# Kernel optimization log

Hardware: AMD Instinct MI355X
Metric: run time of the kernel (lower is better)

The kernel has to match this reference:

```python
import jax, jax.numpy as jnp
import numpy as np

N, K, C0, H = 256, 16, 16, 32  # vertices, regular degree, input feats, hidden


def setup_inputs() -> dict:
    key = jax.random.key(0)
    ks = jax.random.split(key, 4)
    # k-regular circulant graph: neighbors of i are i+/-1..i+/-K//2 (mod N), sorted by vertex id
    offs = np.concatenate([np.arange(1, K // 2 + 1), -np.arange(1, K // 2 + 1)])
    nbrs = np.sort((np.arange(N)[:, None] + offs[None, :]) % N, axis=1).astype(np.int32)
    X = jax.random.normal(ks[0], (N, C0), jnp.float32)
    W1 = jax.random.normal(ks[1], (18 * C0, H), jnp.float32) / np.sqrt(18 * C0)
    b1 = jnp.zeros((H,), jnp.float32)
    W2 = jax.random.normal(ks[2], (18 * H, H), jnp.float32) / np.sqrt(18 * H)
    b2 = jnp.zeros((H,), jnp.float32)
    fc_w = jax.random.normal(ks[3], (H, 1), jnp.float32) / np.sqrt(H)
    fc_b = jnp.zeros((1,), jnp.float32)
    return {"X": X, "nbrs": jnp.asarray(nbrs), "W1": W1, "b1": b1,
            "W2": W2, "b2": b2, "fc_w": fc_w, "fc_b": fc_b}


def contract18(T, A):
    """All 18 contractions of F6[t,a,b,e,f,c] = T[t,a,b,c] * A[e,f],
    exactly matching _collapse6to3 (_c6to2_111 + _c6to2_12 + _c6to2_3),
    without materializing the 6-d tensor.
    T: (n, k, k, k, c) with axes (vertex, t, a, b, channel); A: (k, k).
    Returns (n, k, k, 18*c)."""
    S = A.sum()            # total sum of A
    r = A.sum(1)           # row sums
    tr = jnp.trace(A)
    sum_b = T.sum(3)              # (n,t,a,c)
    sum_t = T.sum(1)              # (n,a,b,c)
    sum_ab = T.sum((2, 3))        # (n,t,c)
    sum_tb = T.sum((1, 3))        # (n,a,c)
    sum_all = T.sum((1, 2, 3))    # (n,c)
    # _c6to2_111 (5 permutations)
    c1 = sum_b * S
    c2 = sum_ab[:, :, None, :] * r[None, None, :, None]
    c3 = sum_t * S
    c4 = sum_tb[:, :, None, :] * r[None, None, :, None]
    c5 = sum_all[:, None, None, :] * A[None, :, :, None]
    # _c6to2_12 (1 nontrivial permutation + 9 identical identity permutations)
    c6 = jnp.einsum('ntabc,b->ntac', T, r)
    c7 = sum_b * tr  # repeated 9 times, as in the source
    # _c6to2_3 (3 planar-diagonal contractions)
    d_ab = jnp.diagonal(T, axis1=2, axis2=3).transpose(0, 1, 3, 2)   # (n,t,a,c): T[t,a,a,c]
    c16 = jnp.einsum('ntac,ea->ntec', d_ab, A)
    d_tb = jnp.diagonal(T, axis1=1, axis2=3)                          # (n,a,c,t): T[t,a,t,c]
    c17 = jnp.einsum('nact,et->naec', d_tb, A)
    d_ttt = jnp.einsum('ntttc->ntc', T).sum(1)                        # (n,c)
    c18 = d_ttt[:, None, None, :] * A[None, :, :, None]
    return jnp.concatenate([c1, c2, c3, c4, c5, c6] + [c7] * 9 + [c16, c17, c18], axis=-1)


def _forward(X, nbrs, W1, b1, W2, b2, fc_w, fc_b):
    n, k = nbrs.shape
    # chi_{i,t}[a,p] = 1 iff a-th neighbor of i == p-th neighbor of j, j = nbrs[i,t]
    NN = nbrs[nbrs]                                                    # (n,k,k)
    CH = (nbrs[:, None, :, None] == NN[:, :, None, :]).astype(X.dtype)  # (n,t,a,p)
    A = jnp.eye(k, dtype=X.dtype)  # chi_{i,i} is the k x k identity for every i

    # get_F0: broadcast vertex features to (n, k, k, c0)
    F = jnp.broadcast_to(X[:, None, None, :], (n, k, k, X.shape[1]))

    def layer(F, W, b):
        Fg = F[nbrs]                                             # (n,t,p,q,c) gather neighbor features
        tmp = jnp.einsum('ntap,ntpqc->ntaqc', CH, Fg)            # chi @ F
        T = jnp.einsum('ntaqc,ntbq->ntabc', tmp, CH)             # (chi @ F) @ chi^T
        col = contract18(T, A)                                   # (n,k,k,18c)
        return jax.nn.relu(col @ W + b)

    F1 = layer(F, W1, b1)
    F2 = layer(F1, W2, b2)
    # get_Troot then full sum: chi_root scatters F2 entries injectively into [n,n,c],
    # so sum over Troot == sum over all entries of F2.
    g = F2.sum((0, 1, 2))                                        # (H,)
    return g @ fc_w + fc_b                                       # (1,)


def reference(X, nbrs, W1, b1, W2, b2, fc_w, fc_b):
    return _forward(X, nbrs, W1, b1, W2, b2, fc_w, fc_b)
```

## Files before the change

kernel.cpp:

```cpp
#include <hip/hip_runtime.h>


constexpr int KN = 16, HH = 32, NV = 256, C2 = 32;

__device__ __forceinline__ float rlane(float v, int l) {
    return __int_as_float(__builtin_amdgcn_readlane(__float_as_int(v), l));
}

#define MM_RL(WPTR, NB, COEF_EXPR, ACC) do {                                   \
    _Pragma("unroll")                                                          \
    for (int B = 0; B < (NB); ++B) {                                           \
        const float4 w_ = ((const float4*)(WPTR))[B * 64 + lane];              \
        _Pragma("unroll")                                                      \
        for (int cc = 0; cc < 8; ++cc) {                                       \
            const int ci = B * 8 + cc;                                         \
            const float cf_ = (COEF_EXPR);                                     \
            _Pragma("unroll")                                                  \
            for (int h4 = 0; h4 < 8; ++h4) {                                   \
                const int src_ = 8 * cc + h4;                                  \
                (ACC)[4*h4+0] = fmaf(cf_, rlane(w_.x, src_), (ACC)[4*h4+0]);   \
                (ACC)[4*h4+1] = fmaf(cf_, rlane(w_.y, src_), (ACC)[4*h4+1]);   \
                (ACC)[4*h4+2] = fmaf(cf_, rlane(w_.z, src_), (ACC)[4*h4+2]);   \
                (ACC)[4*h4+3] = fmaf(cf_, rlane(w_.w, src_), (ACC)[4*h4+3]);   \
            }                                                                  \
        }                                                                      \
    }                                                                          \
} while (0)

__global__ __launch_bounds__(512)
void ccn_l1(const float* __restrict__ X, const int* __restrict__ nbrs,
            const float* __restrict__ W1, const float* __restrict__ bias,
            float* __restrict__ F1c, float* __restrict__ outz)
{
    __shared__ float sE1[6 * 512];
    __shared__ float sPP2[8 * 256 * 4];
    __shared__ float sX[16][20];
    __shared__ float sV[16][164];
    __shared__ int   s_nbi[16];
    __shared__ int   s_nbj[16][17];
    __shared__ int   s_P[16][16];
    __shared__ int   s_vm[16];
    __shared__ float s_m[16];

    const int tid  = threadIdx.x;
    const int i    = ((blockIdx.x & 7) << 5) | (blockIdx.x >> 3);
    const int lane = tid & 63;

    if (blockIdx.x == 0 && tid == 0) outz[0] = 0.f;
    if (tid < 16) s_nbi[tid] = nbrs[i * 16 + tid];
    __syncthreads();

    if (tid < 256) {
        const int t = tid >> 4, y = tid & 15;
        const int j = s_nbi[t];
        s_nbj[t][y] = nbrs[j * 16 + y];
        sX[t][y]    = X[j * 16 + y];
    } else {
        const int u = tid - 256;
        float acc = 0.f;
        #pragma unroll
        for (int g = 6; g < 15; ++g) acc += W1[g * 512 + u];
        sE1[u]        = 16.f * W1[u] + W1[5 * 512 + u] + 16.f * acc;
        sE1[512 + u]  = W1[512 + u];
        sE1[1024 + u] = W1[15 * 512 + u];
        sE1[1536 + u] = 16.f * W1[2 * 512 + u];
        sE1[2048 + u] = W1[3 * 512 + u];
        sE1[2560 + u] = W1[4 * 512 + u];
    }
    __syncthreads();

    if (tid < 256) {
        const int t = tid >> 4, y = tid & 15;
        const int tgt = s_nbi[y];
        int p = -1;
        #pragma unroll
        for (int q = 0; q < 16; ++q) if (s_nbj[t][q] == tgt) p = q;
        s_P[t][y] = p;
        unsigned long long bal = __ballot(p >= 0);
        if (y == 0) {
            int vm = (int)((bal >> ((t & 3) * 16)) & 0xFFFFull);
            s_vm[t] = vm;
            s_m[t]  = (float)__popc(vm);
        }
    } else {
        const int u = tid;
        float acc = 0.f;
        #pragma unroll
        for (int g = 6; g < 15; ++g) acc += W1[g * 512 + u];
        sE1[u]        = 16.f * W1[u] + W1[5 * 512 + u] + 16.f * acc;
        sE1[512 + u]  = W1[512 + u];
        sE1[1024 + u] = W1[15 * 512 + u];
        sE1[1536 + u] = 16.f * W1[2 * 512 + u];
        sE1[2048 + u] = W1[3 * 512 + u];
        sE1[2560 + u] = W1[4 * 512 + u];
    }
    __syncthreads();

    if (tid < 256) {
        const int t = tid >> 4, y = tid & 15, x = t;
        float Y0[16];
        #pragma unroll
        for (int c4 = 0; c4 < 4; ++c4) {
            float4 v = *(const float4*)&sX[t][4 * c4];
            Y0[4*c4+0] = v.x; Y0[4*c4+1] = v.y; Y0[4*c4+2] = v.z; Y0[4*c4+3] = v.w;
        }
        float Z4[16], Z5[16];
        #pragma unroll
        for (int c = 0; c < 16; ++c) { Z4[c] = 0.f; Z5[c] = 0.f; }
        #pragma unroll
        for (int tp = 0; tp < 16; ++tp) {
            const int vm = s_vm[tp];
            const float mt = s_m[tp];
            const float fb = ((vm >> x) & 1) ? mt : 0.f;
            const float f5 = mt * mt;
            #pragma unroll
            for (int c4 = 0; c4 < 4; ++c4) {
                float4 v = *(const float4*)&sX[tp][4 * c4];
                Z4[4*c4+0] = fmaf(fb, v.x, Z4[4*c4+0]);
                Z4[4*c4+1] = fmaf(fb, v.y, Z4[4*c4+1]);
                Z4[4*c4+2] = fmaf(fb, v.z, Z4[4*c4+2]);
                Z4[4*c4+3] = fmaf(fb, v.w, Z4[4*c4+3]);
                Z5[4*c4+0] = fmaf(f5, v.x, Z5[4*c4+0]);
                Z5[4*c4+1] = fmaf(f5, v.y, Z5[4*c4+1]);
                Z5[4*c4+2] = fmaf(f5, v.z, Z5[4*c4+2]);
                Z5[4*c4+3] = fmaf(f5, v.w, Z5[4*c4+3]);
            }
        }
        const float m = s_m[t];
        float v0a=0.f,v0b=0.f,v1a=0.f,v1b=0.f,v2a=0.f,v2b=0.f;
        float v3a=0.f,v3b=0.f,v4a=0.f,v4b=0.f;
        const float2* Wsb = (const float2*)(sE1 + 0 * 512);
        const float2* Wab = (const float2*)(sE1 + 1 * 512);
        const float2* W16 = (const float2*)(sE1 + 2 * 512);
        const float2* Wtb = (const float2*)(sE1 + 4 * 512);
        const float2* Wal = (const float2*)(sE1 + 5 * 512);
        #pragma unroll
        for (int c = 0; c < 16; ++c) {
            const float cf0 = m * Y0[c];
            const float cf1 = m * cf0;
            const float cf2 = Y0[c];
            const float cf3 = Z4[c];
            const float cf4 = Z5[c];
            const int idx = c * 16 + y;
            float2 w0 = Wsb[idx]; v0a = fmaf(cf0, w0.x, v0a); v0b = fmaf(cf0, w0.y, v0b);
            float2 w1 = Wab[idx]; v1a = fmaf(cf1, w1.x, v1a); v1b = fmaf(cf1, w1.y, v1b);
            float2 w2 = W16[idx]; v2a = fmaf(cf2, w2.x, v2a); v2b = fmaf(cf2, w2.y, v2b);
            float2 w3 = Wtb[idx]; v3a = fmaf(cf3, w3.x, v3a); v3b = fmaf(cf3, w3.y, v3b);
            float2 w4 = Wal[idx]; v4a = fmaf(cf4, w4.x, v4a); v4b = fmaf(cf4, w4.y, v4b);
        }
        *(float2*)&sV[t][0 * 32 + 2 * y] = make_float2(v0a, v0b);
        *(float2*)&sV[t][1 * 32 + 2 * y] = make_float2(v1a, v1b);
        *(float2*)&sV[t][2 * 32 + 2 * y] = make_float2(v2a, v2b);
        *(float2*)&sV[t][3 * 32 + 2 * y] = make_float2(v3a, v3b);
        *(float2*)&sV[t][4 * 32 + 2 * y] = make_float2(v4a, v4b);
    } else {
        const int w = tid - 256;
        const int t = w >> 4, y = w & 15, x = t;
        float Z2[16];
        #pragma unroll
        for (int c = 0; c < 16; ++c) Z2[c] = 0.f;
        #pragma unroll
        for (int tp = 0; tp < 16; ++tp) {
            const int vm = s_vm[tp];
            const float f2 = (float)((vm >> x) & (vm >> y) & 1);
            #pragma unroll
            for (int c4 = 0; c4 < 4; ++c4) {
                float4 v = *(const float4*)&sX[tp][4 * c4];
                Z2[4*c4+0] = fmaf(f2, v.x, Z2[4*c4+0]);
                Z2[4*c4+1] = fmaf(f2, v.y, Z2[4*c4+1]);
                Z2[4*c4+2] = fmaf(f2, v.z, Z2[4*c4+2]);
                Z2[4*c4+3] = fmaf(f2, v.w, Z2[4*c4+3]);
            }
        }
        float pp[HH];
        #pragma unroll
        for (int h = 0; h < HH; ++h) pp[h] = 0.f;
        MM_RL(sE1 + 3 * 512, 2, Z2[ci], pp);
        const int cell = y * 16 + t;
        #pragma unroll
        for (int h4 = 0; h4 < 8; ++h4)
            *(float4*)&sPP2[(h4 * 256 + cell) * 4] =
                make_float4(pp[4*h4], pp[4*h4+1], pp[4*h4+2], pp[4*h4+3]);
    }
    __syncthreads();

    if (tid < 256) {
        const int q = tid >> 4, p = tid & 15;
        const float vy  = (s_P[p][q] >= 0) ? 1.f : 0.f;
        const float dxy = (p == q) ? 1.f : 0.f;
        float4* F4 = (float4*)F1c;
        const size_t basec = ((size_t)i * 16 + q) * 128 + p;
        #pragma unroll
        for (int h4 = 0; h4 < 8; ++h4) {
            const float4 V0 = *(const float4*)&sV[p][0 * 32 + 4 * h4];
            const float4 V1 = *(const float4*)&sV[p][1 * 32 + 4 * h4];
            const float4 V2 = *(const float4*)&sV[p][2 * 32 + 4 * h4];
            const float4 V3 = *(const float4*)&sV[p][3 * 32 + 4 * h4];
            const float4 V4 = *(const float4*)&sV[p][4 * 32 + 4 * h4];
            const float4 PP = *(const float4*)&sPP2[(h4 * 256 + q * 16 + p) * 4];
            float a_ = vy*(V0.x+V2.x) + V1.x + V3.x + dxy*V4.x + PP.x + bias[4*h4+0];
            float b_ = vy*(V0.y+V2.y) + V1.y + V3.y + dxy*V4.y + PP.y + bias[4*h4+1];
            float c_ = vy*(V0.z+V2.z) + V1.z + V3.z + dxy*V4.z + PP.z + bias[4*h4+2];
            float d_ = vy*(V0.w+V2.w) + V1.w + V3.w + dxy*V4.w + PP.w + bias[4*h4+3];
            F4[basec + h4 * 16] = make_float4(a_ > 0.f ? a_ : 0.f, b_ > 0.f ? b_ : 0.f,
                                              c_ > 0.f ? c_ : 0.f, d_ > 0.f ? d_ : 0.f);
        }
    }
}

__global__ __launch_bounds__(512)
void ccn_l2(const float* __restrict__ F1c, const int* __restrict__ nbrs,
            const float* __restrict__ W2, const float* __restrict__ bias,
            const float* __restrict__ fcw, const float* __restrict__ fcb,
            float* __restrict__ out)
{
    __shared__ float sE2[6 * 1024];
    __shared__ float sRpp[256 * 36];
    __shared__ float s_stb[16 * 33];
    __shared__ float s_sall[C2];
    __shared__ int   s_nbi[16];
    __shared__ int   s_PQ[16 * 17];
    __shared__ float s_red[4];

    const int tid  = threadIdx.x;
    const int i    = ((blockIdx.x & 7) << 5) | (blockIdx.x >> 3);
    const int lane = tid & 63;
    const float4* F4 = (const float4*)F1c;

    if (tid < 16) s_nbi[tid] = nbrs[i * 16 + tid];
    __syncthreads();

    if (tid < 256) {
        const int t = tid >> 4, y = tid & 15;
        const int j = s_nbi[t];
        s_PQ[t * 17 + y] = nbrs[j * 16 + y];
    } else {
        const int w = tid - 256;
        #pragma unroll
        for (int k = 0; k < 2; ++k) {
            const int u = w + k * 256;
            float acc = 0.f;
            #pragma unroll
            for (int g = 6; g < 15; ++g) acc += W2[g * 1024 + u];
            sE2[u]        = 16.f * W2[u] + W2[5 * 1024 + u] + 16.f * acc;
            sE2[1024 + u] = W2[1024 + u];
            sE2[2048 + u] = W2[15 * 1024 + u];
            sE2[3072 + u] = 16.f * W2[2 * 1024 + u];
            sE2[4096 + u] = W2[3 * 1024 + u];
            sE2[5120 + u] = W2[4 * 1024 + u];
        }
    }
    __syncthreads();

    if (tid < 256) {
        const int t = tid >> 4, y = tid & 15;
        const int tgt = s_nbi[y];
        int p = -1;
        #pragma unroll
        for (int q = 0; q < 16; ++q) if (s_PQ[t * 17 + q] == tgt) p = q;
        s_PQ[t * 17 + y] = p;
    } else {
        const int w = tid - 256;
        #pragma unroll
        for (int k = 2; k < 4; ++k) {
            const int u = w + k * 256;
            float acc = 0.f;
            #pragma unroll
            for (int g = 6; g < 15; ++g) acc += W2[g * 1024 + u];
            sE2[u]        = 16.f * W2[u] + W2[5 * 1024 + u] + 16.f * acc;
            sE2[1024 + u] = W2[1024 + u];
            sE2[2048 + u] = W2[15 * 1024 + u];
            sE2[3072 + u] = 16.f * W2[2 * 1024 + u];
            sE2[4096 + u] = W2[3 * 1024 + u];
            sE2[5120 + u] = W2[4 * 1024 + u];
        }
    }
    __syncthreads();

    float pre[HH];
    float sab[C2];
    float pp[HH];

    if (tid < 256) {
        const int t = tid >> 4, y = tid & 15;
        const int j = s_nbi[t];
        const int p = s_PQ[t * 17 + y];
        const float mp = (p >= 0) ? 1.f : 0.f;
        const int pc = p >= 0 ? p : 0;
        const size_t jbase = (size_t)j * 2048;

        float R[C2];
        #pragma unroll
        for (int c = 0; c < C2; ++c) R[c] = 0.f;
        #pragma unroll
        for (int b = 0; b < 16; ++b) {
            const int q = s_PQ[t * 17 + b];
            const float mm = (q >= 0) ? mp : 0.f;
            const int qc = q >= 0 ? q : 0;
            const size_t rb = jbase + (size_t)qc * 128 + pc;
            #pragma unroll
            for (int c4 = 0; c4 < 8; ++c4) {
                float4 v = F4[rb + c4 * 16];
                R[4*c4+0] = fmaf(mm, v.x, R[4*c4+0]);
                R[4*c4+1] = fmaf(mm, v.y, R[4*c4+1]);
                R[4*c4+2] = fmaf(mm, v.z, R[4*c4+2]);
                R[4*c4+3] = fmaf(mm, v.w, R[4*c4+3]);
            }
        }
        #pragma unroll
        for (int c4 = 0; c4 < 8; ++c4)
            *(float4*)&sRpp[(t * 16 + y) * 36 + 4 * c4] =
                make_float4(R[4*c4+0], R[4*c4+1], R[4*c4+2], R[4*c4+3]);

        #pragma unroll
        for (int h = 0; h < HH; ++h) pre[h] = 0.f;
        MM_RL(sE2 + 0 * 1024, 4, R[ci], pre);

        #pragma unroll
        for (int c = 0; c < C2; ++c) {
            float s = R[c];
            s += __shfl_xor(s, 1);
            s += __shfl_xor(s, 2);
            s += __shfl_xor(s, 4);
            s += __shfl_xor(s, 8);
            sab[c] = s;
        }

        float D[C2];
        {
            const size_t db = jbase + (size_t)pc * 128 + pc;
            #pragma unroll
            for (int c4 = 0; c4 < 8; ++c4) {
                float4 v = F4[db + c4 * 16];
                D[4*c4+0] = mp * v.x; D[4*c4+1] = mp * v.y;
                D[4*c4+2] = mp * v.z; D[4*c4+3] = mp * v.w;
            }
        }
        MM_RL(sE2 + 2 * 1024, 4, D[ci], pre);
    } else {
        const int w = tid - 256;
        const int g = w >> 4, l = w & 15;
        float ST[C2];
        #pragma unroll
        for (int c = 0; c < C2; ++c) ST[c] = 0.f;
        #pragma unroll
        for (int tp = 0; tp < 16; ++tp) {
            const int jt = s_nbi[tp];
            const int py = s_PQ[tp * 17 + g];
            const int px = s_PQ[tp * 17 + l];
            const float mm = (px >= 0 && py >= 0) ? 1.f : 0.f;
            const int pyc = py >= 0 ? py : 0;
            const int pxc = px >= 0 ? px : 0;
            const size_t rb = (size_t)jt * 2048 + (size_t)pyc * 128 + pxc;
            #pragma unroll
            for (int c4 = 0; c4 < 8; ++c4) {
                float4 v = F4[rb + c4 * 16];
                ST[4*c4+0] = fmaf(mm, v.x, ST[4*c4+0]);
                ST[4*c4+1] = fmaf(mm, v.y, ST[4*c4+1]);
                ST[4*c4+2] = fmaf(mm, v.z, ST[4*c4+2]);
                ST[4*c4+3] = fmaf(mm, v.w, ST[4*c4+3]);
            }
        }
        #pragma unroll
        for (int h = 0; h < HH; ++h) pp[h] = 0.f;
        MM_RL(sE2 + 3 * 1024, 4, ST[ci], pp);
    }
    __syncthreads();

    if (tid < 256) {
        #pragma unroll
        for (int k = 0; k < 2; ++k) {
            const int x2 = (tid >> 5) + 8 * k;
            const int c = tid & 31;
            float s = 0.f;
            #pragma unroll
            for (int tt = 0; tt < 16; ++tt) s += sRpp[(tt * 16 + x2) * 36 + c];
            s_stb[x2 * 33 + c] = s;
        }
    }
    __syncthreads();

    if (tid < 256) {
        if (tid < 32) {
            float s = 0.f;
            #pragma unroll
            for (int x2 = 0; x2 < 16; ++x2) s += s_stb[x2 * 33 + tid];
            s_sall[tid] = s;
        }
    } else {
        const int w = tid - 256;
        const int g = w >> 4, l = w & 15;
        float* dst = &sRpp[(l * 16 + g) * 36];
        #pragma unroll
        for (int h4 = 0; h4 < 8; ++h4)
            *(float4*)&dst[4 * h4] = make_float4(pp[4*h4], pp[4*h4+1], pp[4*h4+2], pp[4*h4+3]);
    }
    __syncthreads();

    if (tid < 256) {
        const int t = tid >> 4, y = tid & 15, x = t;
        const float dxy = (x == y) ? 1.f : 0.f;
        float S0 = 0.f, S1 = 0.f, L0 = 0.f, L1 = 0.f;
        {
            const float2* Wab = (const float2*)(sE2 + 1 * 1024);
            const float2* Wtb = (const float2*)(sE2 + 4 * 1024);
            const float2* Wal = (const float2*)(sE2 + 5 * 1024);
            #pragma unroll
            for (int c = 0; c < C2; ++c) {
                const float cfa = sab[c];
                const float cft = s_stb[t * 33 + c];
                const float cfl = s_sall[c];
                const int idx = c * 16 + y;
                float2 wa = Wab[idx]; S0 = fmaf(cfa, wa.x, S0); S1 = fmaf(cfa, wa.y, S1);
                float2 wt = Wtb[idx]; S0 = fmaf(cft, wt.x, S0); S1 = fmaf(cft, wt.y, S1);
                float2 wl = Wal[idx]; L0 = fmaf(cfl, wl.x, L0); L1 = fmaf(cfl, wl.y, L1);
            }
        }
        const int gbase = (t & 3) * 16;
        #pragma unroll
        for (int h = 0; h < HH; ++h) {
            const int src = gbase + (h >> 1);
            const float sv = (h & 1) ? S1 : S0;
            const float lv = (h & 1) ? L1 : L0;
            pre[h] += __shfl(sv, src, 64) + dxy * __shfl(lv, src, 64);
        }
        {
            const float* ppr = &sRpp[(t * 16 + y) * 36];
            #pragma unroll
            for (int h4 = 0; h4 < 8; ++h4) {
                const float4 v = *(const float4*)&ppr[4 * h4];
                pre[4*h4+0] += v.x; pre[4*h4+1] += v.y;
                pre[4*h4+2] += v.z; pre[4*h4+3] += v.w;
            }
        }
        float local = 0.f;
        #pragma unroll
        for (int h = 0; h < HH; ++h) {
            float v = pre[h] + bias[h];
            v = v > 0.f ? v : 0.f;
            local += v * fcw[h];
        }
        #pragma unroll
        for (int off = 32; off > 0; off >>= 1) local += __shfl_down(local, off, 64);
        if (lane == 0) s_red[tid >> 6] = local;
    }
    __syncthreads();
    if (tid == 0) {
        const float v = s_red[0] + s_red[1] + s_red[2] + s_red[3]
                      + fcb[0] * (1.f / 256.f);
        atomicAdd(out, v);
    }
}

extern "C" void kernel_launch(void* const* d_in, const int* in_sizes, int n_in,
                              void* d_out, int out_size, void* d_ws, size_t ws_size,
                              hipStream_t stream) {
    const float* X    = (const float*)d_in[0];
    const int*   nbrs = (const int*)  d_in[1];
    const float* W1   = (const float*)d_in[2];
    const float* b1   = (const float*)d_in[3];
    const float* W2   = (const float*)d_in[4];
    const float* b2   = (const float*)d_in[5];
    const float* fc_w = (const float*)d_in[6];
    const float* fc_b = (const float*)d_in[7];
    float* outp = (float*)d_out;

    float* F1c = (float*)d_ws;

    ccn_l1<<<NV, 512, 0, stream>>>(X, nbrs, W1, b1, F1c, outp);
    ccn_l2<<<NV, 512, 0, stream>>>(F1c, nbrs, W2, b2, fc_w, fc_b, outp);
}
```

Measured before the change: 106.3 us.

## Precompute layer-2 combined weights in layer-1 kernel and read weights directly from global

Blocks 0 and 1 of the first kernel now precompute the summed layer-2 weight matrix into workspace, so each block of the second kernel no longer re-reduces W2 slices into shared memory. The matmul macro now reads weight rows directly from global (uniform float4 loads) in place of staging them in shared memory and broadcasting them with readlane. This cuts shared memory use and per-block setup, at the cost of many more global/L2 weight loads inside the inner products. It relies on kernel ordering on the stream for the workspace dependency.

```diff
diff --git a/kernel.cpp b/kernel.cpp
--- a/kernel.cpp
+++ b/kernel.cpp
@@ -3,25 +3,21 @@
 
 constexpr int KN = 16, HH = 32, NV = 256, C2 = 32;
 
-__device__ __forceinline__ float rlane(float v, int l) {
-    return __int_as_float(__builtin_amdgcn_readlane(__float_as_int(v), l));
-}
-
-#define MM_RL(WPTR, NB, COEF_EXPR, ACC) do {                                   \
+#define MM_SL(WPTR, NB, COEF_EXPR, ACC) do {                                   \
+    const float4* W4_ = (const float4*)(WPTR);                                 \
     _Pragma("unroll")                                                          \
     for (int B = 0; B < (NB); ++B) {                                           \
-        const float4 w_ = ((const float4*)(WPTR))[B * 64 + lane];              \
         _Pragma("unroll")                                                      \
         for (int cc = 0; cc < 8; ++cc) {                                       \
             const int ci = B * 8 + cc;                                         \
             const float cf_ = (COEF_EXPR);                                     \
             _Pragma("unroll")                                                  \
             for (int h4 = 0; h4 < 8; ++h4) {                                   \
-                const int src_ = 8 * cc + h4;                                  \
-                (ACC)[4*h4+0] = fmaf(cf_, rlane(w_.x, src_), (ACC)[4*h4+0]);   \
-                (ACC)[4*h4+1] = fmaf(cf_, rlane(w_.y, src_), (ACC)[4*h4+1]);   \
-                (ACC)[4*h4+2] = fmaf(cf_, rlane(w_.z, src_), (ACC)[4*h4+2]);   \
-                (ACC)[4*h4+3] = fmaf(cf_, rlane(w_.w, src_), (ACC)[4*h4+3]);   \
+                const float4 w_ = W4_[ci * 8 + h4];                            \
+                (ACC)[4*h4+0] = fmaf(cf_, w_.x, (ACC)[4*h4+0]);                \
+                (ACC)[4*h4+1] = fmaf(cf_, w_.y, (ACC)[4*h4+1]);                \
+                (ACC)[4*h4+2] = fmaf(cf_, w_.z, (ACC)[4*h4+2]);                \
+                (ACC)[4*h4+3] = fmaf(cf_, w_.w, (ACC)[4*h4+3]);                \
             }                                                                  \
         }                                                                      \
     }                                                                          \
@@ -30,7 +26,8 @@
 __global__ __launch_bounds__(512)
 void ccn_l1(const float* __restrict__ X, const int* __restrict__ nbrs,
             const float* __restrict__ W1, const float* __restrict__ bias,
-            float* __restrict__ F1c, float* __restrict__ outz)
+            float* __restrict__ F1c, float* __restrict__ outz,
+            const float* __restrict__ W2f, float* __restrict__ Wsb2)
 {
     __shared__ float sE1[6 * 512];
     __shared__ float sPP2[8 * 256 * 4];
@@ -44,9 +41,17 @@
 
     const int tid  = threadIdx.x;
     const int i    = ((blockIdx.x & 7) << 5) | (blockIdx.x >> 3);
-    const int lane = tid & 63;
 
     if (blockIdx.x == 0 && tid == 0) outz[0] = 0.f;
+
+    if (blockIdx.x < 2) {
+        const int u = (blockIdx.x << 9) | tid;
+        float acc = 0.f;
+        #pragma unroll
+        for (int g = 6; g < 15; ++g) acc += W2f[g * 1024 + u];
+        Wsb2[u] = 16.f * W2f[u] + W2f[5 * 1024 + u] + 16.f * acc;
+    }
+
     if (tid < 16) s_nbi[tid] = nbrs[i * 16 + tid];
     __syncthreads();
 
@@ -63,7 +68,6 @@
         sE1[u]        = 16.f * W1[u] + W1[5 * 512 + u] + 16.f * acc;
         sE1[512 + u]  = W1[512 + u];
         sE1[1024 + u] = W1[15 * 512 + u];
-        sE1[1536 + u] = 16.f * W1[2 * 512 + u];
         sE1[2048 + u] = W1[3 * 512 + u];
         sE1[2560 + u] = W1[4 * 512 + u];
     }
@@ -90,7 +94,6 @@
         sE1[u]        = 16.f * W1[u] + W1[5 * 512 + u] + 16.f * acc;
         sE1[512 + u]  = W1[512 + u];
         sE1[1024 + u] = W1[15 * 512 + u];
-        sE1[1536 + u] = 16.f * W1[2 * 512 + u];
         sE1[2048 + u] = W1[3 * 512 + u];
         sE1[2560 + u] = W1[4 * 512 + u];
     }
@@ -175,7 +178,7 @@
         float pp[HH];
         #pragma unroll
         for (int h = 0; h < HH; ++h) pp[h] = 0.f;
-        MM_RL(sE1 + 3 * 512, 2, Z2[ci], pp);
+        MM_SL(W1 + 2 * 512, 2, 16.f * Z2[ci], pp);
         const int cell = y * 16 + t;
         #pragma unroll
         for (int h4 = 0; h4 < 8; ++h4)
@@ -212,9 +215,9 @@
 void ccn_l2(const float* __restrict__ F1c, const int* __restrict__ nbrs,
             const float* __restrict__ W2, const float* __restrict__ bias,
             const float* __restrict__ fcw, const float* __restrict__ fcb,
-            float* __restrict__ out)
+            float* __restrict__ out, const float* __restrict__ Wsb2)
 {
-    __shared__ float sE2[6 * 1024];
+    __shared__ float sW3[3 * 1024];
     __shared__ float sRpp[256 * 36];
     __shared__ float s_stb[16 * 33];
     __shared__ float s_sall[C2];
@@ -237,17 +240,11 @@
     } else {
         const int w = tid - 256;
         #pragma unroll
-        for (int k = 0; k < 2; ++k) {
-            const int u = w + k * 256;
-            float acc = 0.f;
-            #pragma unroll
-            for (int g = 6; g < 15; ++g) acc += W2[g * 1024 + u];
-            sE2[u]        = 16.f * W2[u] + W2[5 * 1024 + u] + 16.f * acc;
-            sE2[1024 + u] = W2[1024 + u];
-            sE2[2048 + u] = W2[15 * 1024 + u];
-            sE2[3072 + u] = 16.f * W2[2 * 1024 + u];
-            sE2[4096 + u] = W2[3 * 1024 + u];
-            sE2[5120 + u] = W2[4 * 1024 + u];
+        for (int s = 0; s < 4; ++s) {
+            const int u = w + s * 256;
+            sW3[u]        = W2[1 * 1024 + u];
+            sW3[1024 + u] = W2[3 * 1024 + u];
+            sW3[2048 + u] = W2[4 * 1024 + u];
         }
     }
     __syncthreads();
@@ -259,21 +256,6 @@
         #pragma unroll
         for (int q = 0; q < 16; ++q) if (s_PQ[t * 17 + q] == tgt) p = q;
         s_PQ[t * 17 + y] = p;
-    } else {
-        const int w = tid - 256;
-        #pragma unroll
-        for (int k = 2; k < 4; ++k) {
-            const int u = w + k * 256;
-            float acc = 0.f;
-            #pragma unroll
-            for (int g = 6; g < 15; ++g) acc += W2[g * 1024 + u];
-            sE2[u]        = 16.f * W2[u] + W2[5 * 1024 + u] + 16.f * acc;
-            sE2[1024 + u] = W2[1024 + u];
-            sE2[2048 + u] = W2[15 * 1024 + u];
-            sE2[3072 + u] = 16.f * W2[2 * 1024 + u];
-            sE2[4096 + u] = W2[3 * 1024 + u];
-            sE2[5120 + u] = W2[4 * 1024 + u];
-        }
     }
     __syncthreads();
 
@@ -314,7 +296,7 @@
 
         #pragma unroll
         for (int h = 0; h < HH; ++h) pre[h] = 0.f;
-        MM_RL(sE2 + 0 * 1024, 4, R[ci], pre);
+        MM_SL(Wsb2, 4, R[ci], pre);
 
         #pragma unroll
         for (int c = 0; c < C2; ++c) {
@@ -336,7 +318,7 @@
                 D[4*c4+2] = mp * v.z; D[4*c4+3] = mp * v.w;
             }
         }
-        MM_RL(sE2 + 2 * 1024, 4, D[ci], pre);
+        MM_SL(W2 + 15 * 1024, 4, D[ci], pre);
     } else {
         const int w = tid - 256;
         const int g = w >> 4, l = w & 15;
@@ -363,7 +345,7 @@
         }
         #pragma unroll
         for (int h = 0; h < HH; ++h) pp[h] = 0.f;
-        MM_RL(sE2 + 3 * 1024, 4, ST[ci], pp);
+        MM_SL(W2 + 2 * 1024, 4, 16.f * ST[ci], pp);
     }
     __syncthreads();
 
@@ -402,9 +384,9 @@
         const float dxy = (x == y) ? 1.f : 0.f;
         float S0 = 0.f, S1 = 0.f, L0 = 0.f, L1 = 0.f;
         {
-            const float2* Wab = (const float2*)(sE2 + 1 * 1024);
-            const float2* Wtb = (const float2*)(sE2 + 4 * 1024);
-            const float2* Wal = (const float2*)(sE2 + 5 * 1024);
+            const float2* Wab = (const float2*)(sW3 + 0 * 1024);
+            const float2* Wtb = (const float2*)(sW3 + 1 * 1024);
+            const float2* Wal = (const float2*)(sW3 + 2 * 1024);
             #pragma unroll
             for (int c = 0; c < C2; ++c) {
                 const float cfa = sab[c];
@@ -465,8 +447,9 @@
     const float* fc_b = (const float*)d_in[7];
     float* outp = (float*)d_out;
 
-    float* F1c = (float*)d_ws;
-
-    ccn_l1<<<NV, 512, 0, stream>>>(X, nbrs, W1, b1, F1c, outp);
-    ccn_l2<<<NV, 512, 0, stream>>>(F1c, nbrs, W2, b2, fc_w, fc_b, outp);
+    float* F1c  = (float*)d_ws;
+    float* Wsb2 = F1c + 2097152;
+
+    ccn_l1<<<NV, 512, 0, stream>>>(X, nbrs, W1, b1, F1c, outp, W2, Wsb2);
+    ccn_l2<<<NV, 512, 0, stream>>>(F1c, nbrs, W2, b2, fc_w, fc_b, outp, Wsb2);
 }
```

Measured after the change: 113.6 us. 6.8% more time.
